# Kernel tuning notes

Measured on AMD Instinct MI355X. Metric: run time of the kernel, lower is better.

Reference implementation:

```python
import jax, jax.numpy as jnp
import numpy as np

N = 100000      # nodes
E = 3200000     # edges
IN = 64         # in_channels
OUT = 256       # out_channels (hidden)
OSZ = 4         # output_size


def setup_inputs() -> dict:
    key = jax.random.key(0)
    ks = jax.random.split(key, 16)
    s = 0.05
    inp = {
        "x": jax.random.normal(ks[0], (N, IN), jnp.float32),
        "edge_index": jax.random.randint(ks[1], (2, E), 0, N, jnp.int64),
        # GCNConv weights for z, r, h gates: [IN, OUT] + bias [OUT]
        "Wz": jax.random.normal(ks[2], (IN, OUT), jnp.float32) * s,
        "bz": jnp.zeros((OUT,), jnp.float32),
        "Wr": jax.random.normal(ks[3], (IN, OUT), jnp.float32) * s,
        "br": jnp.zeros((OUT,), jnp.float32),
        "Wh": jax.random.normal(ks[4], (IN, OUT), jnp.float32) * s,
        "bh": jnp.zeros((OUT,), jnp.float32),
        # GRU linear layers: [2*OUT, OUT] + bias [OUT]
        "Lzw": jax.random.normal(ks[5], (2 * OUT, OUT), jnp.float32) * s,
        "Lzb": jnp.zeros((OUT,), jnp.float32),
        "Lrw": jax.random.normal(ks[6], (2 * OUT, OUT), jnp.float32) * s,
        "Lrb": jnp.zeros((OUT,), jnp.float32),
        "Lhw": jax.random.normal(ks[7], (2 * OUT, OUT), jnp.float32) * s,
        "Lhb": jnp.zeros((OUT,), jnp.float32),
        # output head
        "Wo": jax.random.normal(ks[8], (OUT, OSZ), jnp.float32) * s,
        "bo": jnp.zeros((OSZ,), jnp.float32),
    }
    return inp


def _gcn_conv(x, W, b, src, dst, n):
    # GCNConv with symmetric normalization and self-loops (fill_value=1):
    # out = D^{-1/2}(A+I)D^{-1/2} X W + b
    ones = jnp.ones_like(src, dtype=x.dtype)
    deg = jax.ops.segment_sum(ones, dst, num_segments=n) + 1.0  # +1 for self-loop
    dinv = jax.lax.rsqrt(deg)                                   # [N]
    norm = dinv[src] * dinv[dst]                                # [E]
    agg = jax.ops.segment_sum(x[src] * norm[:, None], dst, num_segments=n)
    agg = agg + x * (dinv * dinv)[:, None]                      # self-loop term
    return agg @ W + b


def reference(x, edge_index, Wz, bz, Wr, br, Wh, bh,
              Lzw, Lzb, Lrw, Lrb, Lhw, Lhb, Wo, bo):
    src, dst = edge_index[0], edge_index[1]
    n = x.shape[0]
    H = jnp.zeros((n, Wz.shape[1]), x.dtype)  # TGCN initial hidden state
    # update gate
    Z = jax.nn.sigmoid(jnp.concatenate([_gcn_conv(x, Wz, bz, src, dst, n), H], 1) @ Lzw + Lzb)
    # reset gate
    R = jax.nn.sigmoid(jnp.concatenate([_gcn_conv(x, Wr, br, src, dst, n), H], 1) @ Lrw + Lrb)
    # candidate state
    Ht = jnp.tanh(jnp.concatenate([_gcn_conv(x, Wh, bh, src, dst, n), H * R], 1) @ Lhw + Lhb)
    H = Z * H + (1.0 - Z) * Ht
    # head: ReLU -> Linear -> Softmax(dim=1)
    h = jax.nn.relu(H)
    return jax.nn.softmax(h @ Wo + bo, axis=1)
```

## Files before the change

kernel.cpp:

```cpp
#include <hip/hip_runtime.h>
#include <hip/hip_fp16.h>


#define SHIFT 7
#define NPB   128
#define BMAX  1024
#define TILE  8192
#define EPT   16
#define MBBLK 64
#define CAPB  5120

typedef __attribute__((ext_vector_type(8))) short short8;
typedef __attribute__((ext_vector_type(4))) float floatx4;

__device__ __forceinline__ ushort f2b(float f) {
    union { float f; unsigned u; } v; v.f = f;
    unsigned r = v.u + 0x7FFFu + ((v.u >> 16) & 1u);
    return (ushort)(r >> 16);
}

__device__ __forceinline__ float fastrcp(float x) {
    return __builtin_amdgcn_rcpf(x);
}

__global__ __launch_bounds__(512) void scatter_build_kernel(
    const int* __restrict__ srcs, const int* __restrict__ dsts,
    int* __restrict__ gcur, int* __restrict__ staging, int E, int B, int nT,
    const float* __restrict__ Wz, const float* __restrict__ bz,
    const float* __restrict__ Wh, const float* __restrict__ bh,
    const float* __restrict__ Lzw, const float* __restrict__ Lzb,
    const float* __restrict__ Lhw, const float* __restrict__ Lhb,
    ushort* __restrict__ Mb, float* __restrict__ cb) {
    __shared__ int cnt[BMAX];
    __shared__ int ssum[BMAX];
    __shared__ int gbase[BMAX];
    __shared__ int cur[BMAX];
    __shared__ int sorted[TILE];
    if (blockIdx.x < nT) {
        int tid = threadIdx.x;
        for (int i = tid; i < BMAX; i += 512) cnt[i] = 0;
        __syncthreads();
        int tile0 = blockIdx.x * TILE;
        int dreg[EPT];
#pragma unroll
        for (int j = 0; j < EPT; ++j) {
            int e = tile0 + j * 512 + tid;
            dreg[j] = (e < E) ? dsts[e] : -1;
            if (dreg[j] >= 0) atomicAdd(&cnt[((unsigned)dreg[j]) >> SHIFT], 1);
        }
        __syncthreads();
        {
            int i0 = tid, i1 = tid + 512;
            ssum[i0] = cnt[i0];
            ssum[i1] = cnt[i1];
            __syncthreads();
            for (int off = 1; off < BMAX; off <<= 1) {
                int t0 = (i0 >= off) ? ssum[i0 - off] : 0;
                int t1 = (i1 >= off) ? ssum[i1 - off] : 0;
                __syncthreads();
                ssum[i0] += t0;
                ssum[i1] += t1;
                __syncthreads();
            }
        }
        for (int i = tid; i < BMAX; i += 512) {
            int c = cnt[i];
            gbase[i] = (c > 0) ? atomicAdd(&gcur[i], c) : 0;
            cur[i] = ssum[i] - c;
        }
        __syncthreads();
#pragma unroll
        for (int j = 0; j < EPT; ++j) {
            int d = dreg[j];
            if (d >= 0) {
                int e = tile0 + j * 512 + tid;
                int s = srcs[e];
                int b = ((unsigned)d) >> SHIFT;
                int pos = atomicAdd(&cur[b], 1);
                sorted[pos] = ((d & (NPB - 1)) << 17) | s;
            }
        }
        __syncthreads();
        int grp = tid >> 4, l16 = tid & 15;
        for (int b = grp; b < B; b += 32) {
            int c = cnt[b];
            if (c == 0) continue;
            int lb = ssum[b] - c;
            int gb = gbase[b];
            size_t gp = (size_t)b * CAPB + gb;
            for (int j = l16; j < c; j += 16)
                if (gb + j < CAPB) staging[gp + j] = sorted[lb + j];
        }
    } else {
        int j = (blockIdx.x - nT) * 8 + (threadIdx.x >> 6);
        int k = threadIdx.x & 63;
        int which = j >> 8;
        int jj = j & 255;
        const float* W  = which ? Wh  : Wz;
        const float* bv = which ? bh  : bz;
        const float* L  = which ? Lhw : Lzw;
        const float* Lb = which ? Lhb : Lzb;
        const float4* Wr = (const float4*)(W + k * 256);
        float acc = 0.f;
        for (int t4 = 0; t4 < 64; ++t4) {
            float4 wv = Wr[t4];
            int t = t4 * 4;
            acc = fmaf(wv.x, L[(t + 0) * 256 + jj], acc);
            acc = fmaf(wv.y, L[(t + 1) * 256 + jj], acc);
            acc = fmaf(wv.z, L[(t + 2) * 256 + jj], acc);
            acc = fmaf(wv.w, L[(t + 3) * 256 + jj], acc);
        }
        Mb[j * 64 + k] = f2b(acc);
        if (k == 0) {
            float a = 0.f;
            for (int t = 0; t < 256; ++t) a = fmaf(bv[t], L[t * 256 + jj], a);
            cb[j] = a + Lb[jj];
        }
    }
}

__global__ __launch_bounds__(512) void prep_kernel(const int* __restrict__ staging,
                                                   const int* __restrict__ gcur,
                                                   const float* __restrict__ x,
                                                   int* __restrict__ deg,
                                                   __half* __restrict__ xs,
                                                   int n, int B) {
    int b = blockIdx.x;
    int tid = threadIdx.x;
    __shared__ int nd[NPB];
    __shared__ float sdinv[NPB];
    if (tid < NPB) nd[tid] = 0;
    __syncthreads();
    int count = gcur[b];
    if (count > CAPB) count = CAPB;
    size_t base = (size_t)b * CAPB;
    for (int i = tid; i < count; i += 512)
        atomicAdd(&nd[staging[base + i] >> 17], 1);
    __syncthreads();
    if (tid < NPB) {
        int dg = nd[tid];
        float dn = rsqrtf((float)dg + 1.0f);
        sdinv[tid] = dn;
        int node = (b << SHIFT) + tid;
        if (node < n) deg[node] = dg;
    }
    __syncthreads();
    int nbase = b << SHIFT;
    for (int i2 = tid; i2 < NPB * 16; i2 += 512) {
        int nl = i2 >> 4;
        int node = nbase + nl;
        if (node < n) {
            float dn = sdinv[nl];
            size_t gi = (size_t)node * 16 + (i2 & 15);
            float4 vx = ((const float4*)x)[gi];
            __half2 a = __floats2half2_rn(vx.x * dn, vx.y * dn);
            __half2 c = __floats2half2_rn(vx.z * dn, vx.w * dn);
            ((__half2*)xs)[gi * 2 + 0] = a;
            ((__half2*)xs)[gi * 2 + 1] = c;
        }
    }
}

__global__ __launch_bounds__(512) void bucket_gather_kernel(
    const int* __restrict__ staging,
    const int* __restrict__ gcur,
    const int* __restrict__ deg,
    const __half* __restrict__ xs,
    ushort* __restrict__ aggb, int n, int B) {
    int b   = blockIdx.x;
    int tid = threadIdx.x;
    __shared__ int   csrl[CAPB];
    __shared__ int   sstart[NPB];
    __shared__ int   ncur[NPB];
    __shared__ int   sdeg[NPB];
    __shared__ int   ssc[NPB];
    __shared__ float sdinv[NPB];
    int node0 = b << SHIFT;
    int count = gcur[b];
    if (count > CAPB) count = CAPB;
    size_t base = (size_t)b * CAPB;
    if (tid < NPB) {
        int nodeid = node0 + tid;
        int dg = (nodeid < n) ? deg[nodeid] : 0;
        sdeg[tid] = dg;
        ssc[tid]  = dg;
        sdinv[tid] = rsqrtf((float)dg + 1.0f);
    }
    __syncthreads();
    for (int off = 1; off < NPB; off <<= 1) {
        int t = 0;
        if (tid < NPB && tid >= off) t = ssc[tid - off];
        __syncthreads();
        if (tid < NPB) ssc[tid] += t;
        __syncthreads();
    }
    if (tid < NPB) {
        int excl = ssc[tid] - sdeg[tid];
        sstart[tid] = excl;
        ncur[tid]   = excl;
    }
    __syncthreads();
    for (int i = tid; i < count; i += 512) {
        int p = staging[base + i];
        int pos = atomicAdd(&ncur[p >> 17], 1);
        if (pos < CAPB) csrl[pos] = p & 0x1FFFF;
    }
    __syncthreads();
    int wv = tid >> 6, lane = tid & 63;
    int eg = lane >> 3;
    int c  = lane & 7;
    for (int t16 = 0; t16 < 16; ++t16) {
        int nl   = (wv << 4) + t16;
        int node = node0 + nl;
        int s0 = sstart[nl];
        int d  = sdeg[nl];
        __half2 hz = __float2half2_rn(0.f);
        __half2 hacc[4] = {hz, hz, hz, hz};
        int full = d & ~15;
        for (int be = 0; be < full; be += 16) {
            int qb = s0 + be;
            if (qb > CAPB - 16) qb = CAPB - 16;
            int i0 = csrl[qb + eg];
            int i1 = csrl[qb + 8 + eg];
            union { uint4 u; __half2 h[4]; } p0, p1;
            p0.u = *(const uint4*)(xs + (size_t)i0 * 64 + c * 8);
            p1.u = *(const uint4*)(xs + (size_t)i1 * 64 + c * 8);
#pragma unroll
            for (int t = 0; t < 4; ++t) hacc[t] = __hadd2(hacc[t], p0.h[t]);
#pragma unroll
            for (int t = 0; t < 4; ++t) hacc[t] = __hadd2(hacc[t], p1.h[t]);
        }
        if (full < d) {
            int e0 = full + eg;
            int e1 = full + 8 + eg;
            int q0 = s0 + (e0 < d ? e0 : d - 1);
            int q1 = s0 + (e1 < d ? e1 : d - 1);
            if (q0 > CAPB - 1) q0 = CAPB - 1;
            if (q1 > CAPB - 1) q1 = CAPB - 1;
            int i0 = csrl[q0];
            int i1 = csrl[q1];
            union { uint4 u; __half2 h[4]; } p0, p1;
            p0.u = *(const uint4*)(xs + (size_t)i0 * 64 + c * 8);
            p1.u = *(const uint4*)(xs + (size_t)i1 * 64 + c * 8);
            if (e0 >= d) p0.u = make_uint4(0u, 0u, 0u, 0u);
            if (e1 >= d) p1.u = make_uint4(0u, 0u, 0u, 0u);
#pragma unroll
            for (int t = 0; t < 4; ++t) hacc[t] = __hadd2(hacc[t], p0.h[t]);
#pragma unroll
            for (int t = 0; t < 4; ++t) hacc[t] = __hadd2(hacc[t], p1.h[t]);
        }
#pragma unroll
        for (int off = 32; off >= 8; off >>= 1) {
#pragma unroll
            for (int t = 0; t < 4; ++t) {
                union { __half2 h; int i; } u;
                u.h = hacc[t];
                u.i = __shfl_down(u.i, off);
                hacc[t] = __hadd2(hacc[t], u.h);
            }
        }
        if (eg == 0 && node < n) {
            float dn = sdinv[nl];
            union { uint4 u; __half2 h[4]; } p;
            p.u = *(const uint4*)(xs + (size_t)node * 64 + c * 8);
            uint4 o;
            unsigned* ow = (unsigned*)&o;
#pragma unroll
            for (int t = 0; t < 4; ++t) {
                float2 a = __half22float2(hacc[t]);
                float2 f = __half22float2(p.h[t]);
                float v0 = dn * fmaf(f.x, dn, a.x);
                float v1 = dn * fmaf(f.y, dn, a.y);
                ow[t] = (unsigned)f2b(v0) | ((unsigned)f2b(v1) << 16);
            }
            ((uint4*)(aggb + (size_t)node * 64))[c] = o;
        }
    }
}

__global__ __launch_bounds__(512) void node_mfma_kernel(
    const ushort* __restrict__ aggb,
    const ushort* __restrict__ Mb,
    const float* __restrict__ cb,
    const float* __restrict__ Wo, const float* __restrict__ bo,
    float* __restrict__ out, int n) {
    int tid  = threadIdx.x;
    int w    = tid >> 6;
    int lane = tid & 63;
    int nidx = lane & 15;
    int quad = lane >> 4;
    short8 bfz[2][2], bfh[2][2];
    float cbz[2], cbh[2];
#pragma unroll
    for (int cg = 0; cg < 2; ++cg) {
        int colZ = (w << 5) + (cg << 4) + nidx;
        int colH = 256 + colZ;
#pragma unroll
        for (int s = 0; s < 2; ++s) {
            bfz[cg][s] = *(const short8*)(Mb + colZ * 64 + s * 32 + quad * 8);
            bfh[cg][s] = *(const short8*)(Mb + colH * 64 + s * 32 + quad * 8);
        }
        cbz[cg] = cb[colZ];
        cbh[cg] = cb[colH];
    }
    __shared__ float sH[32][260];
    __shared__ float sWo[4][256];
    if (tid < 256) {
#pragma unroll
        for (int o = 0; o < 4; ++o) sWo[o][tid] = Wo[tid * 4 + o];
    }
    float bo0 = bo[0], bo1 = bo[1], bo2 = bo[2], bo3 = bo[3];
    int ntiles = (n + 31) >> 5;
    for (int tile = blockIdx.x; tile < ntiles; tile += gridDim.x) {
        int node0 = tile << 5;
        int nA0 = node0 + nidx;
        int nA1 = node0 + 16 + nidx;
        if (nA0 >= n) nA0 = n - 1;
        if (nA1 >= n) nA1 = n - 1;
        const ushort* ar0 = aggb + (size_t)nA0 * 64;
        const ushort* ar1 = aggb + (size_t)nA1 * 64;
        short8 a00 = *(const short8*)(ar0 + quad * 8);
        short8 a01 = *(const short8*)(ar0 + 32 + quad * 8);
        short8 a10 = *(const short8*)(ar1 + quad * 8);
        short8 a11 = *(const short8*)(ar1 + 32 + quad * 8);
#pragma unroll
        for (int cg = 0; cg < 2; ++cg) {
            int col = (w << 5) + (cg << 4) + nidx;
#pragma unroll
            for (int grp = 0; grp < 2; ++grp) {
                short8 a0 = grp ? a10 : a00;
                short8 a1 = grp ? a11 : a01;
                floatx4 cz = {cbz[cg], cbz[cg], cbz[cg], cbz[cg]};
                cz = __builtin_amdgcn_mfma_f32_16x16x32_bf16(a0, bfz[cg][0], cz, 0, 0, 0);
                cz = __builtin_amdgcn_mfma_f32_16x16x32_bf16(a1, bfz[cg][1], cz, 0, 0, 0);
                floatx4 chh = {cbh[cg], cbh[cg], cbh[cg], cbh[cg]};
                chh = __builtin_amdgcn_mfma_f32_16x16x32_bf16(a0, bfh[cg][0], chh, 0, 0, 0);
                chh = __builtin_amdgcn_mfma_f32_16x16x32_bf16(a1, bfh[cg][1], chh, 0, 0, 0);
#pragma unroll
                for (int r = 0; r < 4; ++r) {
                    int row = (grp << 4) + (quad << 2) + r;
                    float zc = fastrcp(1.0f + __expf(cz[r]));
                    float th = 1.0f - 2.0f * fastrcp(1.0f + __expf(2.0f * chh[r]));
                    sH[row][col] = fmaxf(zc * th, 0.0f);
                }
            }
        }
        __syncthreads();
        {
            int nb = tid >> 4, g = tid & 15;
            float l0 = 0.f, l1 = 0.f, l2 = 0.f, l3 = 0.f;
#pragma unroll
            for (int ii = 0; ii < 16; ++ii) {
                int ch = g + 16 * ii;
                float hv = sH[nb][ch];
                l0 = fmaf(hv, sWo[0][ch], l0);
                l1 = fmaf(hv, sWo[1][ch], l1);
                l2 = fmaf(hv, sWo[2][ch], l2);
                l3 = fmaf(hv, sWo[3][ch], l3);
            }
#pragma unroll
            for (int off = 8; off > 0; off >>= 1) {
                l0 += __shfl_down(l0, off, 16);
                l1 += __shfl_down(l1, off, 16);
                l2 += __shfl_down(l2, off, 16);
                l3 += __shfl_down(l3, off, 16);
            }
            int node = node0 + nb;
            if (g == 0 && node < n) {
                float v0 = l0 + bo0, v1 = l1 + bo1, v2 = l2 + bo2, v3 = l3 + bo3;
                float mx = fmaxf(fmaxf(v0, v1), fmaxf(v2, v3));
                float e0 = __expf(v0 - mx), e1 = __expf(v1 - mx);
                float e2 = __expf(v2 - mx), e3 = __expf(v3 - mx);
                float inv = fastrcp(e0 + e1 + e2 + e3);
                float4 o;
                o.x = e0 * inv; o.y = e1 * inv; o.z = e2 * inv; o.w = e3 * inv;
                ((float4*)out)[node] = o;
            }
        }
        __syncthreads();
    }
}

extern "C" void kernel_launch(void* const* d_in, const int* in_sizes, int n_in,
                              void* d_out, int out_size, void* d_ws, size_t ws_size,
                              hipStream_t stream) {
    const float* x   = (const float*)d_in[0];
    const int*  eidx = (const int*)d_in[1];
    const float* Wz  = (const float*)d_in[2];
    const float* bz  = (const float*)d_in[3];
    const float* Wh  = (const float*)d_in[6];
    const float* bh  = (const float*)d_in[7];
    const float* Lzw = (const float*)d_in[8];
    const float* Lzb = (const float*)d_in[9];
    const float* Lhw = (const float*)d_in[12];
    const float* Lhb = (const float*)d_in[13];
    const float* Wo  = (const float*)d_in[14];
    const float* bo  = (const float*)d_in[15];
    float* out = (float*)d_out;

    int n = in_sizes[0] / 64;
    int E = in_sizes[1] / 2;
    const int* srcs = eidx;
    const int* dsts = eidx + E;
    int B = (n + NPB - 1) >> SHIFT;
    int nT = (E + TILE - 1) / TILE;

    size_t na = ((size_t)n + 3) & ~(size_t)3;
    size_t stageBytes = (((size_t)B * CAPB * 4) + 255) & ~(size_t)255;
    size_t aggBytes   = (((size_t)n * 64 * 2) + 255) & ~(size_t)255;

    char* ws = (char*)d_ws;
    int*   deg   = (int*)ws;    ws += na * 4;
    int*   gcur  = (int*)ws;    ws += BMAX * 4;
    int*   staging = (int*)ws;  ws += stageBytes;
    __half* xs   = (__half*)ws; ws += (size_t)n * 64 * 2;
    ushort* aggb = (ushort*)ws; ws += aggBytes;
    ushort* Mb   = (ushort*)ws; ws += 512 * 64 * 2;
    float* cb    = (float*)ws;  ws += 512 * 4;

    hipMemsetAsync(gcur, 0, BMAX * 4, stream);
    scatter_build_kernel<<<nT + MBBLK, 512, 0, stream>>>(srcs, dsts, gcur,
                                                         staging, E, B, nT,
                                                         Wz, bz, Wh, bh,
                                                         Lzw, Lzb, Lhw, Lhb,
                                                         Mb, cb);
    prep_kernel<<<B, 512, 0, stream>>>(staging, gcur, x, deg, xs, n, B);
    bucket_gather_kernel<<<B, 512, 0, stream>>>(staging, gcur, deg,
                                                xs, aggb, n, B);
    node_mfma_kernel<<<1024, 512, 0, stream>>>(aggb, Mb, cb, Wo, bo, out, n);
}
```

Before: 238.4 us.

## Split gather into feature quarters mapped to XCDs and precompute bucket CSR

The prep kernel now also sorts each bucket's edges into a local CSR and writes it to global memory. It stores the scaled half-precision features in four column-quarter planes. The gather kernel launches four times as many blocks, and each block handles one feature quarter for one node bucket. Block IDs are mapped so each quarter lands on a pair of XCDs, which is meant to shrink each XCD's gathered working set and improve L2 hit rate. The cost is re-reading the CSR once per quarter, extra global traffic for the CSR array, and smaller 32-byte gathers per edge.

```diff
diff --git a/kernel.cpp b/kernel.cpp
--- a/kernel.cpp
+++ b/kernel.cpp
@@ -119,16 +119,21 @@
     }
 }
 
-__global__ __launch_bounds__(512) void prep_kernel(const int* __restrict__ staging,
-                                                   const int* __restrict__ gcur,
-                                                   const float* __restrict__ x,
-                                                   int* __restrict__ deg,
-                                                   __half* __restrict__ xs,
-                                                   int n, int B) {
+__global__ __launch_bounds__(512) void prep_sort_kernel(
+    const int* __restrict__ staging,
+    const int* __restrict__ gcur,
+    const float* __restrict__ x,
+    int* __restrict__ deg,
+    int* __restrict__ csr,
+    __half* __restrict__ xsq,
+    int n, int B) {
     int b = blockIdx.x;
     int tid = threadIdx.x;
-    __shared__ int nd[NPB];
+    __shared__ int   nd[NPB];
+    __shared__ int   ssc[NPB];
+    __shared__ int   ncur[NPB];
     __shared__ float sdinv[NPB];
+    __shared__ int   csrl[CAPB];
     if (tid < NPB) nd[tid] = 0;
     __syncthreads();
     int count = gcur[b];
@@ -137,41 +142,64 @@
     for (int i = tid; i < count; i += 512)
         atomicAdd(&nd[staging[base + i] >> 17], 1);
     __syncthreads();
+    int d0 = 0;
+    if (tid < NPB) { d0 = nd[tid]; ssc[tid] = d0; }
+    __syncthreads();
+    for (int off = 1; off < NPB; off <<= 1) {
+        int t = 0;
+        if (tid < NPB && tid >= off) t = ssc[tid - off];
+        __syncthreads();
+        if (tid < NPB) ssc[tid] += t;
+        __syncthreads();
+    }
     if (tid < NPB) {
-        int dg = nd[tid];
-        float dn = rsqrtf((float)dg + 1.0f);
+        ncur[tid] = ssc[tid] - d0;
+        float dn = rsqrtf((float)d0 + 1.0f);
         sdinv[tid] = dn;
         int node = (b << SHIFT) + tid;
-        if (node < n) deg[node] = dg;
-    }
-    __syncthreads();
+        if (node < n) deg[node] = d0;
+    }
+    __syncthreads();
+    for (int i = tid; i < count; i += 512) {
+        int p = staging[base + i];
+        int pos = atomicAdd(&ncur[p >> 17], 1);
+        if (pos < CAPB) csrl[pos] = p & 0x1FFFF;
+    }
+    __syncthreads();
+    for (int i = tid; i < count; i += 512)
+        csr[base + i] = csrl[i];
     int nbase = b << SHIFT;
     for (int i2 = tid; i2 < NPB * 16; i2 += 512) {
         int nl = i2 >> 4;
+        int g  = i2 & 15;
         int node = nbase + nl;
         if (node < n) {
             float dn = sdinv[nl];
-            size_t gi = (size_t)node * 16 + (i2 & 15);
-            float4 vx = ((const float4*)x)[gi];
-            __half2 a = __floats2half2_rn(vx.x * dn, vx.y * dn);
-            __half2 c = __floats2half2_rn(vx.z * dn, vx.w * dn);
-            ((__half2*)xs)[gi * 2 + 0] = a;
-            ((__half2*)xs)[gi * 2 + 1] = c;
-        }
-    }
-}
-
-__global__ __launch_bounds__(512) void bucket_gather_kernel(
-    const int* __restrict__ staging,
+            float4 vx = ((const float4*)x)[(size_t)node * 16 + g];
+            __half2 a  = __floats2half2_rn(vx.x * dn, vx.y * dn);
+            __half2 c2 = __floats2half2_rn(vx.z * dn, vx.w * dn);
+            int q = g >> 2;
+            size_t off = ((size_t)q * n + node) * 16 + (size_t)(g & 3) * 4;
+            *(__half2*)(xsq + off)     = a;
+            *(__half2*)(xsq + off + 2) = c2;
+        }
+    }
+}
+
+__global__ __launch_bounds__(512) void quarter_gather_kernel(
+    const int* __restrict__ csr,
     const int* __restrict__ gcur,
     const int* __restrict__ deg,
-    const __half* __restrict__ xs,
+    const __half* __restrict__ xsq,
     ushort* __restrict__ aggb, int n, int B) {
-    int b   = blockIdx.x;
+    int blk = blockIdx.x;
+    int xcd = blk & 7;
+    int q   = xcd >> 1;
+    int b   = ((blk >> 3) << 1) | (xcd & 1);
+    if (b >= B) return;
     int tid = threadIdx.x;
     __shared__ int   csrl[CAPB];
     __shared__ int   sstart[NPB];
-    __shared__ int   ncur[NPB];
     __shared__ int   sdeg[NPB];
     __shared__ int   ssc[NPB];
     __shared__ float sdinv[NPB];
@@ -194,21 +222,14 @@
         if (tid < NPB) ssc[tid] += t;
         __syncthreads();
     }
-    if (tid < NPB) {
-        int excl = ssc[tid] - sdeg[tid];
-        sstart[tid] = excl;
-        ncur[tid]   = excl;
-    }
-    __syncthreads();
-    for (int i = tid; i < count; i += 512) {
-        int p = staging[base + i];
-        int pos = atomicAdd(&ncur[p >> 17], 1);
-        if (pos < CAPB) csrl[pos] = p & 0x1FFFF;
-    }
-    __syncthreads();
+    if (tid < NPB) sstart[tid] = ssc[tid] - sdeg[tid];
+    for (int i = tid; i < count; i += 512)
+        csrl[i] = csr[base + i];
+    __syncthreads();
+    const __half* xq = xsq + (size_t)q * n * 16;
     int wv = tid >> 6, lane = tid & 63;
-    int eg = lane >> 3;
-    int c  = lane & 7;
+    int eg = lane >> 1;
+    int c  = lane & 1;
     for (int t16 = 0; t16 < 16; ++t16) {
         int nl   = (wv << 4) + t16;
         int node = node0 + nl;
@@ -216,41 +237,17 @@
         int d  = sdeg[nl];
         __half2 hz = __float2half2_rn(0.f);
         __half2 hacc[4] = {hz, hz, hz, hz};
-        int full = d & ~15;
-        for (int be = 0; be < full; be += 16) {
-            int qb = s0 + be;
-            if (qb > CAPB - 16) qb = CAPB - 16;
-            int i0 = csrl[qb + eg];
-            int i1 = csrl[qb + 8 + eg];
-            union { uint4 u; __half2 h[4]; } p0, p1;
-            p0.u = *(const uint4*)(xs + (size_t)i0 * 64 + c * 8);
-            p1.u = *(const uint4*)(xs + (size_t)i1 * 64 + c * 8);
-#pragma unroll
-            for (int t = 0; t < 4; ++t) hacc[t] = __hadd2(hacc[t], p0.h[t]);
-#pragma unroll
-            for (int t = 0; t < 4; ++t) hacc[t] = __hadd2(hacc[t], p1.h[t]);
-        }
-        if (full < d) {
-            int e0 = full + eg;
-            int e1 = full + 8 + eg;
-            int q0 = s0 + (e0 < d ? e0 : d - 1);
-            int q1 = s0 + (e1 < d ? e1 : d - 1);
-            if (q0 > CAPB - 1) q0 = CAPB - 1;
-            if (q1 > CAPB - 1) q1 = CAPB - 1;
-            int i0 = csrl[q0];
-            int i1 = csrl[q1];
-            union { uint4 u; __half2 h[4]; } p0, p1;
-            p0.u = *(const uint4*)(xs + (size_t)i0 * 64 + c * 8);
-            p1.u = *(const uint4*)(xs + (size_t)i1 * 64 + c * 8);
-            if (e0 >= d) p0.u = make_uint4(0u, 0u, 0u, 0u);
-            if (e1 >= d) p1.u = make_uint4(0u, 0u, 0u, 0u);
-#pragma unroll
-            for (int t = 0; t < 4; ++t) hacc[t] = __hadd2(hacc[t], p0.h[t]);
-#pragma unroll
-            for (int t = 0; t < 4; ++t) hacc[t] = __hadd2(hacc[t], p1.h[t]);
-        }
-#pragma unroll
-        for (int off = 32; off >= 8; off >>= 1) {
+        for (int be = 0; be < d; be += 32) {
+            int e = be + eg;
+            int idx = csrl[s0 + (e < d ? e : d - 1)];
+            union { uint4 u; __half2 h[4]; } p;
+            p.u = *(const uint4*)(xq + (size_t)idx * 16 + c * 8);
+            if (e >= d) p.u = make_uint4(0u, 0u, 0u, 0u);
+#pragma unroll
+            for (int t = 0; t < 4; ++t) hacc[t] = __hadd2(hacc[t], p.h[t]);
+        }
+#pragma unroll
+        for (int off = 2; off <= 32; off <<= 1) {
 #pragma unroll
             for (int t = 0; t < 4; ++t) {
                 union { __half2 h; int i; } u;
@@ -262,7 +259,7 @@
         if (eg == 0 && node < n) {
             float dn = sdinv[nl];
             union { uint4 u; __half2 h[4]; } p;
-            p.u = *(const uint4*)(xs + (size_t)node * 64 + c * 8);
+            p.u = *(const uint4*)(xq + (size_t)node * 16 + c * 8);
             uint4 o;
             unsigned* ow = (unsigned*)&o;
 #pragma unroll
@@ -273,7 +270,7 @@
                 float v1 = dn * fmaf(f.y, dn, a.y);
                 ow[t] = (unsigned)f2b(v0) | ((unsigned)f2b(v1) << 16);
             }
-            ((uint4*)(aggb + (size_t)node * 64))[c] = o;
+            *(uint4*)(aggb + (size_t)node * 64 + q * 16 + c * 8) = o;
         }
     }
 }
@@ -406,14 +403,15 @@
     int nT = (E + TILE - 1) / TILE;
 
     size_t na = ((size_t)n + 3) & ~(size_t)3;
-    size_t stageBytes = (((size_t)B * CAPB * 4) + 255) & ~(size_t)255;
-    size_t aggBytes   = (((size_t)n * 64 * 2) + 255) & ~(size_t)255;
+    size_t bucketArr = (((size_t)B * CAPB * 4) + 255) & ~(size_t)255;
+    size_t aggBytes  = (((size_t)n * 64 * 2) + 255) & ~(size_t)255;
 
     char* ws = (char*)d_ws;
     int*   deg   = (int*)ws;    ws += na * 4;
     int*   gcur  = (int*)ws;    ws += BMAX * 4;
-    int*   staging = (int*)ws;  ws += stageBytes;
-    __half* xs   = (__half*)ws; ws += (size_t)n * 64 * 2;
+    int*   staging = (int*)ws;  ws += bucketArr;
+    int*   csr   = (int*)ws;    ws += bucketArr;
+    __half* xsq  = (__half*)ws; ws += (size_t)n * 64 * 2;
     ushort* aggb = (ushort*)ws; ws += aggBytes;
     ushort* Mb   = (ushort*)ws; ws += 512 * 64 * 2;
     float* cb    = (float*)ws;  ws += 512 * 4;
@@ -424,8 +422,10 @@
                                                          Wz, bz, Wh, bh,
                                                          Lzw, Lzb, Lhw, Lhb,
                                                          Mb, cb);
-    prep_kernel<<<B, 512, 0, stream>>>(staging, gcur, x, deg, xs, n, B);
-    bucket_gather_kernel<<<B, 512, 0, stream>>>(staging, gcur, deg,
-                                                xs, aggb, n, B);
+    prep_sort_kernel<<<B, 512, 0, stream>>>(staging, gcur, x, deg, csr, xsq,
+                                            n, B);
+    int gq = 8 * ((B + 1) / 2);
+    quarter_gather_kernel<<<gq, 512, 0, stream>>>(csr, gcur, deg, xsq,
+                                                  aggb, n, B);
     node_mfma_kernel<<<1024, 512, 0, stream>>>(aggb, Mb, cb, Wo, bo, out, n);
 }
```

New measurement: 309.0 us. +29.6%, slower.
